# Kernel optimization log

Hardware: AMD Instinct MI355X
Metric: run time of the kernel (lower is better)

Reference implementation:

```python
import jax, jax.numpy as jnp
import numpy as np

B, C_IN, C_OUT, H, W = 8, 64, 64, 128, 128
G, K, PAD = 8, 3, 1
CG_OUT = C_OUT // G   # 8
CG_IN = C_IN // G     # 8


def setup_inputs() -> dict:
    key = jax.random.key(0)
    ks = jax.random.split(key, 6)
    x = jax.random.normal(ks[0], (B, C_IN, H, W), dtype=jnp.float32)
    # grouped 1x1 conv weights, stored as (groups, out_per_group, in_per_group)
    scale = (2.0 / C_OUT) ** 0.5  # kaiming fan_out
    Wq = jax.random.normal(ks[1], (G, CG_OUT, CG_IN), dtype=jnp.float32) * scale
    Wk = jax.random.normal(ks[2], (G, CG_OUT, CG_IN), dtype=jnp.float32) * scale
    Wv = jax.random.normal(ks[3], (G, CG_OUT, CG_IN), dtype=jnp.float32) * scale
    h_emb = jax.random.normal(ks[4], (G, CG_OUT // 2, 1, 1, K, 1), dtype=jnp.float32)
    w_emb = jax.random.normal(ks[5], (G, CG_OUT // 2, 1, 1, 1, K), dtype=jnp.float32)
    return {"x": x, "Wq": Wq, "Wk": Wk, "Wv": Wv, "h_emb": h_emb, "w_emb": w_emb}


def _gconv1x1(x, Wt):
    # grouped 1x1 conv: x (B,C,H,W) -> (B,G,Cg,H,W)
    b, c, h, w = x.shape
    xg = x.reshape(b, G, c // G, h, w)
    return jnp.einsum('bgihw,goi->bgohw', xg, Wt)


def _unfold(t):
    # t: (B,G,Cg,H+2p,W+2p) -> (B,G,Cg,H,W,K*K), window index = i*K + j (h-major,
    # matching torch unfold(2).unfold(3).view)
    slices = [t[..., i:i + H, j:j + W] for i in range(K) for j in range(K)]
    return jnp.stack(slices, axis=-1)


def reference(x, Wq, Wk, Wv, h_emb, w_emb):
    x_pad = jnp.pad(x, ((0, 0), (0, 0), (PAD, PAD), (PAD, PAD)))
    q = _gconv1x1(x, Wq)            # (B,G,Cg,H,W)
    kf = _gconv1x1(x_pad, Wk)       # (B,G,Cg,H+2,W+2)
    vf = _gconv1x1(x_pad, Wv)
    kp = _unfold(kf)                # (B,G,Cg,H,W,K^2)
    vp = _unfold(vf)
    # relative position embedding: h half broadcast over w, w half over h
    he = jnp.broadcast_to(h_emb, (G, CG_OUT // 2, 1, 1, K, K))
    we = jnp.broadcast_to(w_emb, (G, CG_OUT // 2, 1, 1, K, K))
    emb = jnp.concatenate([he, we], axis=1).reshape(G, CG_OUT, 1, 1, K * K)
    logits = q[..., None] * (kp + emb[None])       # (B,G,Cg,H,W,K^2)
    attn = jax.nn.softmax(logits, axis=-1)
    out = jnp.sum(attn * vp, axis=-1)              # (B,G,Cg,H,W)
    return out.reshape(x.shape[0], C_OUT, H, W)
```

## Files before the change

### kernel.cpp

```cpp
#include <hip/hip_runtime.h>


typedef float v2f __attribute__((ext_vector_type(2)));
typedef float v4f __attribute__((ext_vector_type(4)));

#define HH 128
#define WW 128
#define HW (HH * WW)
#define PT 34
#define PTS 38
#define LOG2E 1.44269504088896f

__device__ __forceinline__ float sload(float v) {
    return __uint_as_float(__builtin_amdgcn_readfirstlane(__float_as_uint(v)));
}

__global__ __launch_bounds__(256, 5) void sab_fused(
    const float* __restrict__ x,
    const float* __restrict__ Wq,
    const float* __restrict__ Wk,
    const float* __restrict__ Wv,
    const float* __restrict__ h_emb,
    const float* __restrict__ w_emb,
    float* __restrict__ out)
{
    __shared__ v2f kv[2][PT][PTS];

    const int bid0 = blockIdx.x;
    const int work = (bid0 & 7) * 512 + (bid0 >> 3);
    const int c0   = (work & 3) << 1;
    const int tile = (work >> 2) & 15;
    const int bg   = work >> 6;
    const int g    = bg & 7;
    const int h0   = (tile >> 2) << 5;
    const int w0   = (tile & 3) << 5;
    const int tid  = threadIdx.x;
    const int ty   = tid >> 3;
    const int x0   = (tid & 7) << 2;

    float wk[2][8], wv[2][8], wq[2][8], eb[2][9];
    #pragma unroll
    for (int cc = 0; cc < 2; cc++) {
        const int c = c0 + cc;
        #pragma unroll
        for (int i = 0; i < 8; i++) {
            wk[cc][i] = sload(Wk[g * 64 + c * 8 + i]);
            wv[cc][i] = sload(Wv[g * 64 + c * 8 + i]);
            wq[cc][i] = sload(Wq[g * 64 + c * 8 + i]);
        }
        #pragma unroll
        for (int p = 0; p < 9; p++) {
            eb[cc][p] = sload((c < 4) ? h_emb[(g * 4 + c) * 3 + p / 3]
                                      : w_emb[(g * 4 + c - 4) * 3 + p % 3]);
        }
    }

    const float* xb = x + (size_t)bg * 8 * HW;
    const int ibase = (h0 + ty) * WW + (w0 + x0);

    v4f xi[8];
    #pragma unroll
    for (int i = 0; i < 8; i++)
        xi[i] = *reinterpret_cast<const v4f*>(xb + i * HW + ibase);

    v4f kk0 = 0.f, vv0 = 0.f, qq0 = 0.f, kk1 = 0.f, vv1 = 0.f, qq1 = 0.f;
    #pragma unroll
    for (int i = 0; i < 8; i++) {
        const v4f xv = xi[i];
        kk0 += wk[0][i] * xv;  vv0 += wv[0][i] * xv;  qq0 += wq[0][i] * xv;
        kk1 += wk[1][i] * xv;  vv1 += wv[1][i] * xv;  qq1 += wq[1][i] * xv;
    }
    #pragma unroll
    for (int px = 0; px < 4; px++) {
        kv[0][ty + 1][x0 + 1 + px] = (v2f){kk0[px], vv0[px]};
        kv[1][ty + 1][x0 + 1 + px] = (v2f){kk1[px], vv1[px]};
    }
    float q[2][4];
    #pragma unroll
    for (int px = 0; px < 4; px++) {
        q[0][px] = qq0[px] * LOG2E;
        q[1][px] = qq1[px] * LOG2E;
    }

    if (tid < 132) {
        int hpy, hpx;
        if (tid < 34)       { hpy = 0;        hpx = tid; }
        else if (tid < 68)  { hpy = 33;       hpx = tid - 34; }
        else if (tid < 100) { hpy = tid - 67; hpx = 0; }
        else                { hpy = tid - 99; hpx = 33; }
        const int gh = h0 + hpy - 1, gw = w0 + hpx - 1;
        const bool ok = (gh >= 0) & (gh < HH) & (gw >= 0) & (gw < WW);
        const int base = gh * WW + gw;
        float hk0 = 0.f, hv0 = 0.f, hk1 = 0.f, hv1 = 0.f;
        #pragma unroll
        for (int i = 0; i < 8; i++) {
            const float xv = ok ? xb[i * HW + base] : 0.0f;
            hk0 = fmaf(wk[0][i], xv, hk0);
            hv0 = fmaf(wv[0][i], xv, hv0);
            hk1 = fmaf(wk[1][i], xv, hk1);
            hv1 = fmaf(wv[1][i], xv, hv1);
        }
        kv[0][hpy][hpx] = (v2f){hk0, hv0};
        kv[1][hpy][hpx] = (v2f){hk1, hv1};
    }
    __syncthreads();

    float s[2][4] = {{0.f,0.f,0.f,0.f},{0.f,0.f,0.f,0.f}};
    float o[2][4] = {{0.f,0.f,0.f,0.f},{0.f,0.f,0.f,0.f}};
    #pragma unroll
    for (int dh = 0; dh < 3; dh++) {
        #pragma unroll
        for (int cc = 0; cc < 2; cc++) {
            const v2f* row = &kv[cc][ty + dh][x0];
            const v4f a  = *reinterpret_cast<const v4f*>(row);
            const v4f bq = *reinterpret_cast<const v4f*>(row + 2);
            const v4f cq = *reinterpret_cast<const v4f*>(row + 4);
            const float kw[6] = {a.x, a.z, bq.x, bq.z, cq.x, cq.z};
            const float vw[6] = {a.y, a.w, bq.y, bq.w, cq.y, cq.w};
            #pragma unroll
            for (int px = 0; px < 4; px++) {
                const float ql = q[cc][px];
                #pragma unroll
                for (int dw = 0; dw < 3; dw++) {
                    const float e = __builtin_amdgcn_exp2f(
                        ql * (kw[px + dw] + eb[cc][dh * 3 + dw]));
                    s[cc][px] += e;
                    o[cc][px] = fmaf(e, vw[px + dw], o[cc][px]);
                }
            }
        }
    }

    v4f r0, r1;
    #pragma unroll
    for (int px = 0; px < 4; px++) {
        r0[px] = o[0][px] * __builtin_amdgcn_rcpf(s[0][px]);
        r1[px] = o[1][px] * __builtin_amdgcn_rcpf(s[1][px]);
    }
    *reinterpret_cast<v4f*>(out + (size_t)(bg * 8 + c0 + 0) * HW + ibase) = r0;
    *reinterpret_cast<v4f*>(out + (size_t)(bg * 8 + c0 + 1) * HW + ibase) = r1;
}

extern "C" void kernel_launch(void* const* d_in, const int* in_sizes, int n_in,
                              void* d_out, int out_size, void* d_ws, size_t ws_size,
                              hipStream_t stream) {
    const float* x    = (const float*)d_in[0];
    const float* Wq   = (const float*)d_in[1];
    const float* Wk   = (const float*)d_in[2];
    const float* Wv   = (const float*)d_in[3];
    const float* h_e  = (const float*)d_in[4];
    const float* w_e  = (const float*)d_in[5];
    float* out = (float*)d_out;

    dim3 grid(8 * 8 * 16 * 4);
    dim3 block(256);
    sab_fused<<<grid, block, 0, stream>>>(x, Wq, Wk, Wv, h_e, w_e, out);
}
```

Baseline: 28.06 us.

## Use full-width 8-row tiles with planar K/V shared-memory layout

Changes each block's tile from 32x32 to 8 rows by the full 128-pixel width, so only top and bottom halo rows need recomputing and the left/right halo disappears (handled as zero padding at the image edge). K and V move from interleaved float2 to separate planar float arrays, so stores and center loads become 16-byte vectors and halo loads are coalesced v4f reads by 64 threads. The cost is a larger halo fraction per tile (2 rows per 8 instead of a ring per 32x32) and extra scalar LDS loads for the left and right neighbours.

```diff
diff --git a/kernel.cpp b/kernel.cpp
--- a/kernel.cpp
+++ b/kernel.cpp
@@ -1,14 +1,12 @@
 #include <hip/hip_runtime.h>
 
 
-typedef float v2f __attribute__((ext_vector_type(2)));
 typedef float v4f __attribute__((ext_vector_type(4)));
 
 #define HH 128
 #define WW 128
 #define HW (HH * WW)
-#define PT 34
-#define PTS 38
+#define LSTR 132
 #define LOG2E 1.44269504088896f
 
 __device__ __forceinline__ float sload(float v) {
@@ -24,7 +22,8 @@
     const float* __restrict__ w_emb,
     float* __restrict__ out)
 {
-    __shared__ v2f kv[2][PT][PTS];
+    __shared__ float kpl[2][10][LSTR];
+    __shared__ float vpl[2][10][LSTR];
 
     const int bid0 = blockIdx.x;
     const int work = (bid0 & 7) * 512 + (bid0 >> 3);
@@ -32,11 +31,10 @@
     const int tile = (work >> 2) & 15;
     const int bg   = work >> 6;
     const int g    = bg & 7;
-    const int h0   = (tile >> 2) << 5;
-    const int w0   = (tile & 3) << 5;
+    const int h0   = tile << 3;
     const int tid  = threadIdx.x;
-    const int ty   = tid >> 3;
-    const int x0   = (tid & 7) << 2;
+    const int ty   = tid >> 5;
+    const int x0   = (tid & 31) << 2;
 
     float wk[2][8], wv[2][8], wq[2][8], eb[2][9];
     #pragma unroll
@@ -56,7 +54,7 @@
     }
 
     const float* xb = x + (size_t)bg * 8 * HW;
-    const int ibase = (h0 + ty) * WW + (w0 + x0);
+    const int ibase = (h0 + ty) * WW + x0;
 
     v4f xi[8];
     #pragma unroll
@@ -70,56 +68,54 @@
         kk0 += wk[0][i] * xv;  vv0 += wv[0][i] * xv;  qq0 += wq[0][i] * xv;
         kk1 += wk[1][i] * xv;  vv1 += wv[1][i] * xv;  qq1 += wq[1][i] * xv;
     }
-    #pragma unroll
-    for (int px = 0; px < 4; px++) {
-        kv[0][ty + 1][x0 + 1 + px] = (v2f){kk0[px], vv0[px]};
-        kv[1][ty + 1][x0 + 1 + px] = (v2f){kk1[px], vv1[px]};
-    }
-    float q[2][4];
-    #pragma unroll
-    for (int px = 0; px < 4; px++) {
-        q[0][px] = qq0[px] * LOG2E;
-        q[1][px] = qq1[px] * LOG2E;
-    }
+    *reinterpret_cast<v4f*>(&kpl[0][ty + 1][x0]) = kk0;
+    *reinterpret_cast<v4f*>(&vpl[0][ty + 1][x0]) = vv0;
+    *reinterpret_cast<v4f*>(&kpl[1][ty + 1][x0]) = kk1;
+    *reinterpret_cast<v4f*>(&vpl[1][ty + 1][x0]) = vv1;
+    const v4f q0 = qq0 * LOG2E;
+    const v4f q1 = qq1 * LOG2E;
 
-    if (tid < 132) {
-        int hpy, hpx;
-        if (tid < 34)       { hpy = 0;        hpx = tid; }
-        else if (tid < 68)  { hpy = 33;       hpx = tid - 34; }
-        else if (tid < 100) { hpy = tid - 67; hpx = 0; }
-        else                { hpy = tid - 99; hpx = 33; }
-        const int gh = h0 + hpy - 1, gw = w0 + hpx - 1;
-        const bool ok = (gh >= 0) & (gh < HH) & (gw >= 0) & (gw < WW);
-        const int base = gh * WW + gw;
-        float hk0 = 0.f, hv0 = 0.f, hk1 = 0.f, hv1 = 0.f;
-        #pragma unroll
-        for (int i = 0; i < 8; i++) {
-            const float xv = ok ? xb[i * HW + base] : 0.0f;
-            hk0 = fmaf(wk[0][i], xv, hk0);
-            hv0 = fmaf(wv[0][i], xv, hv0);
-            hk1 = fmaf(wk[1][i], xv, hk1);
-            hv1 = fmaf(wv[1][i], xv, hv1);
+    if (tid < 64) {
+        const int hr  = tid >> 5;
+        const int hx0 = (tid & 31) << 2;
+        const int gh  = h0 - 1 + hr * 9;
+        const int lr  = hr * 9;
+        v4f hk0 = 0.f, hv0 = 0.f, hk1 = 0.f, hv1 = 0.f;
+        if (gh >= 0 && gh < HH) {
+            const int base = gh * WW + hx0;
+            #pragma unroll
+            for (int i = 0; i < 8; i++) {
+                const v4f xv = *reinterpret_cast<const v4f*>(xb + i * HW + base);
+                hk0 += wk[0][i] * xv;  hv0 += wv[0][i] * xv;
+                hk1 += wk[1][i] * xv;  hv1 += wv[1][i] * xv;
+            }
         }
-        kv[0][hpy][hpx] = (v2f){hk0, hv0};
-        kv[1][hpy][hpx] = (v2f){hk1, hv1};
+        *reinterpret_cast<v4f*>(&kpl[0][lr][hx0]) = hk0;
+        *reinterpret_cast<v4f*>(&vpl[0][lr][hx0]) = hv0;
+        *reinterpret_cast<v4f*>(&kpl[1][lr][hx0]) = hk1;
+        *reinterpret_cast<v4f*>(&vpl[1][lr][hx0]) = hv1;
     }
     __syncthreads();
 
     float s[2][4] = {{0.f,0.f,0.f,0.f},{0.f,0.f,0.f,0.f}};
     float o[2][4] = {{0.f,0.f,0.f,0.f},{0.f,0.f,0.f,0.f}};
+
     #pragma unroll
-    for (int dh = 0; dh < 3; dh++) {
+    for (int cc = 0; cc < 2; cc++) {
         #pragma unroll
-        for (int cc = 0; cc < 2; cc++) {
-            const v2f* row = &kv[cc][ty + dh][x0];
-            const v4f a  = *reinterpret_cast<const v4f*>(row);
-            const v4f bq = *reinterpret_cast<const v4f*>(row + 2);
-            const v4f cq = *reinterpret_cast<const v4f*>(row + 4);
-            const float kw[6] = {a.x, a.z, bq.x, bq.z, cq.x, cq.z};
-            const float vw[6] = {a.y, a.w, bq.y, bq.w, cq.y, cq.w};
+        for (int dh = 0; dh < 3; dh++) {
+            const int lr = ty + dh;
+            const v4f Bk = *reinterpret_cast<const v4f*>(&kpl[cc][lr][x0]);
+            const v4f Bv = *reinterpret_cast<const v4f*>(&vpl[cc][lr][x0]);
+            const float kL = x0        ? kpl[cc][lr][x0 - 1] : 0.f;
+            const float vL = x0        ? vpl[cc][lr][x0 - 1] : 0.f;
+            const float kR = (x0 < 124) ? kpl[cc][lr][x0 + 4] : 0.f;
+            const float vR = (x0 < 124) ? vpl[cc][lr][x0 + 4] : 0.f;
+            const float kw[6] = {kL, Bk.x, Bk.y, Bk.z, Bk.w, kR};
+            const float vw[6] = {vL, Bv.x, Bv.y, Bv.z, Bv.w, vR};
             #pragma unroll
             for (int px = 0; px < 4; px++) {
-                const float ql = q[cc][px];
+                const float ql = (cc ? q1 : q0)[px];
                 #pragma unroll
                 for (int dw = 0; dw < 3; dw++) {
                     const float e = __builtin_amdgcn_exp2f(
```

After: 82.44 us. 2.94x slower.

## Reshape spatial tile to 16x64 with vectorized halo-row computation

Applied to the files above, without the earlier changes.

Changes each block's spatial tile from 32x32 to 16 rows by 64 columns and resizes the shared K/V buffer to match. The top and bottom halo rows are now computed by 32 threads using float4 loads, and the side columns and corners are handled by 36 scalar threads, replacing the earlier 132-thread scalar halo path. The launch-bounds occupancy hint of 5 is removed. The aim is coalesced, vectorized halo loads with fewer divergent scalar accesses, in exchange for a larger halo perimeter per tile and possibly different register allocation now that the occupancy hint is gone.

```diff
diff --git a/kernel.cpp b/kernel.cpp
--- a/kernel.cpp
+++ b/kernel.cpp
@@ -7,15 +7,14 @@
 #define HH 128
 #define WW 128
 #define HW (HH * WW)
-#define PT 34
-#define PTS 38
+#define PTS 70
 #define LOG2E 1.44269504088896f
 
 __device__ __forceinline__ float sload(float v) {
     return __uint_as_float(__builtin_amdgcn_readfirstlane(__float_as_uint(v)));
 }
 
-__global__ __launch_bounds__(256, 5) void sab_fused(
+__global__ __launch_bounds__(256) void sab_fused(
     const float* __restrict__ x,
     const float* __restrict__ Wq,
     const float* __restrict__ Wk,
@@ -24,7 +23,7 @@
     const float* __restrict__ w_emb,
     float* __restrict__ out)
 {
-    __shared__ v2f kv[2][PT][PTS];
+    __shared__ v2f kv[2][18][PTS];
 
     const int bid0 = blockIdx.x;
     const int work = (bid0 & 7) * 512 + (bid0 >> 3);
@@ -32,11 +31,11 @@
     const int tile = (work >> 2) & 15;
     const int bg   = work >> 6;
     const int g    = bg & 7;
-    const int h0   = (tile >> 2) << 5;
-    const int w0   = (tile & 3) << 5;
+    const int h0   = (tile >> 1) << 4;
+    const int w0   = (tile & 1) << 6;
     const int tid  = threadIdx.x;
-    const int ty   = tid >> 3;
-    const int x0   = (tid & 7) << 2;
+    const int ty   = tid >> 4;
+    const int x0   = (tid & 15) << 2;
 
     float wk[2][8], wv[2][8], wq[2][8], eb[2][9];
     #pragma unroll
@@ -75,20 +74,42 @@
         kv[0][ty + 1][x0 + 1 + px] = (v2f){kk0[px], vv0[px]};
         kv[1][ty + 1][x0 + 1 + px] = (v2f){kk1[px], vv1[px]};
     }
-    float q[2][4];
-    #pragma unroll
-    for (int px = 0; px < 4; px++) {
-        q[0][px] = qq0[px] * LOG2E;
-        q[1][px] = qq1[px] * LOG2E;
-    }
+    const v4f q0 = qq0 * LOG2E;
+    const v4f q1 = qq1 * LOG2E;
 
-    if (tid < 132) {
-        int hpy, hpx;
-        if (tid < 34)       { hpy = 0;        hpx = tid; }
-        else if (tid < 68)  { hpy = 33;       hpx = tid - 34; }
-        else if (tid < 100) { hpy = tid - 67; hpx = 0; }
-        else                { hpy = tid - 99; hpx = 33; }
-        const int gh = h0 + hpy - 1, gw = w0 + hpx - 1;
+    if (tid < 32) {
+        const int hr  = tid >> 4;
+        const int t   = tid & 15;
+        const int gh  = hr ? (h0 + 16) : (h0 - 1);
+        const int lr  = hr ? 17 : 0;
+        const int gw  = w0 + (t << 2);
+        v4f hk0 = 0.f, hv0 = 0.f, hk1 = 0.f, hv1 = 0.f;
+        if (gh >= 0 && gh < HH) {
+            const int base = gh * WW + gw;
+            #pragma unroll
+            for (int i = 0; i < 8; i++) {
+                const v4f xv = *reinterpret_cast<const v4f*>(xb + i * HW + base);
+                hk0 += wk[0][i] * xv;  hv0 += wv[0][i] * xv;
+                hk1 += wk[1][i] * xv;  hv1 += wv[1][i] * xv;
+            }
+        }
+        #pragma unroll
+        for (int px = 0; px < 4; px++) {
+            kv[0][lr][1 + (t << 2) + px] = (v2f){hk0[px], hv0[px]};
+            kv[1][lr][1 + (t << 2) + px] = (v2f){hk1[px], hv1[px]};
+        }
+    } else if (tid < 68) {
+        int hpy, hpx, gh, gw;
+        if (tid < 48)      { hpy = 1 + (tid - 32); hpx = 0;  gh = h0 + (tid - 32); gw = w0 - 1; }
+        else if (tid < 64) { hpy = 1 + (tid - 48); hpx = 65; gh = h0 + (tid - 48); gw = w0 + 64; }
+        else {
+            const int t = tid - 64;
+            const int cy = t >> 1, cx = t & 1;
+            hpy = cy ? 17 : 0;
+            hpx = cx ? 65 : 0;
+            gh  = cy ? (h0 + 16) : (h0 - 1);
+            gw  = cx ? (w0 + 64) : (w0 - 1);
+        }
         const bool ok = (gh >= 0) & (gh < HH) & (gw >= 0) & (gw < WW);
         const int base = gh * WW + gw;
         float hk0 = 0.f, hv0 = 0.f, hk1 = 0.f, hv1 = 0.f;
@@ -119,7 +140,7 @@
             const float vw[6] = {a.y, a.w, bq.y, bq.w, cq.y, cq.w};
             #pragma unroll
             for (int px = 0; px < 4; px++) {
-                const float ql = q[cc][px];
+                const float ql = (cc ? q1 : q0)[px];
                 #pragma unroll
                 for (int dw = 0; dw < 3; dw++) {
                     const float e = __builtin_amdgcn_exp2f(
```

Result: slower. 30.78 us (+9.7%).

## Process four output channels per block with double-buffered k/v tiles

Applied to the files above, without the earlier changes.

Each block now handles four output channels instead of two, halving the grid. It reuses the loaded x tile and halo values across both channel pairs, so x reads from global memory are halved. The k/v computation for the second pair is interleaved with the softmax of the first pair through a double-buffered shared-memory tile. In exchange it uses twice the LDS, more registers, and drops the occupancy hint from launch bounds, which may reduce waves per CU.

```diff
diff --git a/kernel.cpp b/kernel.cpp
--- a/kernel.cpp
+++ b/kernel.cpp
@@ -7,7 +7,6 @@
 #define HH 128
 #define WW 128
 #define HW (HH * WW)
-#define PT 34
 #define PTS 38
 #define LOG2E 1.44269504088896f
 
@@ -15,7 +14,7 @@
     return __uint_as_float(__builtin_amdgcn_readfirstlane(__float_as_uint(v)));
 }
 
-__global__ __launch_bounds__(256, 5) void sab_fused(
+__global__ __launch_bounds__(256) void sab_fused(
     const float* __restrict__ x,
     const float* __restrict__ Wq,
     const float* __restrict__ Wk,
@@ -24,13 +23,13 @@
     const float* __restrict__ w_emb,
     float* __restrict__ out)
 {
-    __shared__ v2f kv[2][PT][PTS];
+    __shared__ v2f kv[2][2][34][PTS];
 
     const int bid0 = blockIdx.x;
-    const int work = (bid0 & 7) * 512 + (bid0 >> 3);
-    const int c0   = (work & 3) << 1;
-    const int tile = (work >> 2) & 15;
-    const int bg   = work >> 6;
+    const int work = (bid0 & 7) * 256 + (bid0 >> 3);
+    const int c0   = (work & 1) << 2;
+    const int tile = (work >> 1) & 15;
+    const int bg   = work >> 5;
     const int g    = bg & 7;
     const int h0   = (tile >> 2) << 5;
     const int w0   = (tile & 3) << 5;
@@ -38,107 +37,203 @@
     const int ty   = tid >> 3;
     const int x0   = (tid & 7) << 2;
 
-    float wk[2][8], wv[2][8], wq[2][8], eb[2][9];
+    const float* xb = x + (size_t)bg * 8 * HW;
+    const int ibase = (h0 + ty) * WW + (w0 + x0);
+
+    float wkA[2][8], wvA[2][8], wqA[2][8], ebA[2][9];
     #pragma unroll
     for (int cc = 0; cc < 2; cc++) {
         const int c = c0 + cc;
         #pragma unroll
         for (int i = 0; i < 8; i++) {
-            wk[cc][i] = sload(Wk[g * 64 + c * 8 + i]);
-            wv[cc][i] = sload(Wv[g * 64 + c * 8 + i]);
-            wq[cc][i] = sload(Wq[g * 64 + c * 8 + i]);
-        }
-        #pragma unroll
-        for (int p = 0; p < 9; p++) {
-            eb[cc][p] = sload((c < 4) ? h_emb[(g * 4 + c) * 3 + p / 3]
-                                      : w_emb[(g * 4 + c - 4) * 3 + p % 3]);
-        }
-    }
-
-    const float* xb = x + (size_t)bg * 8 * HW;
-    const int ibase = (h0 + ty) * WW + (w0 + x0);
+            wkA[cc][i] = sload(Wk[g * 64 + c * 8 + i]);
+            wvA[cc][i] = sload(Wv[g * 64 + c * 8 + i]);
+            wqA[cc][i] = sload(Wq[g * 64 + c * 8 + i]);
+        }
+        #pragma unroll
+        for (int p = 0; p < 9; p++)
+            ebA[cc][p] = sload((c < 4) ? h_emb[(g * 4 + c) * 3 + p / 3]
+                                       : w_emb[(g * 4 + c - 4) * 3 + p % 3]);
+    }
 
     v4f xi[8];
     #pragma unroll
     for (int i = 0; i < 8; i++)
         xi[i] = *reinterpret_cast<const v4f*>(xb + i * HW + ibase);
 
-    v4f kk0 = 0.f, vv0 = 0.f, qq0 = 0.f, kk1 = 0.f, vv1 = 0.f, qq1 = 0.f;
-    #pragma unroll
-    for (int i = 0; i < 8; i++) {
-        const v4f xv = xi[i];
-        kk0 += wk[0][i] * xv;  vv0 += wv[0][i] * xv;  qq0 += wq[0][i] * xv;
-        kk1 += wk[1][i] * xv;  vv1 += wv[1][i] * xv;  qq1 += wq[1][i] * xv;
-    }
-    #pragma unroll
-    for (int px = 0; px < 4; px++) {
-        kv[0][ty + 1][x0 + 1 + px] = (v2f){kk0[px], vv0[px]};
-        kv[1][ty + 1][x0 + 1 + px] = (v2f){kk1[px], vv1[px]};
-    }
-    float q[2][4];
-    #pragma unroll
-    for (int px = 0; px < 4; px++) {
-        q[0][px] = qq0[px] * LOG2E;
-        q[1][px] = qq1[px] * LOG2E;
-    }
-
-    if (tid < 132) {
-        int hpy, hpx;
+    int hpy = 0, hpx = 0;
+    const bool is_halo = tid < 132;
+    if (is_halo) {
         if (tid < 34)       { hpy = 0;        hpx = tid; }
         else if (tid < 68)  { hpy = 33;       hpx = tid - 34; }
         else if (tid < 100) { hpy = tid - 67; hpx = 0; }
         else                { hpy = tid - 99; hpx = 33; }
-        const int gh = h0 + hpy - 1, gw = w0 + hpx - 1;
-        const bool ok = (gh >= 0) & (gh < HH) & (gw >= 0) & (gw < WW);
-        const int base = gh * WW + gw;
-        float hk0 = 0.f, hv0 = 0.f, hk1 = 0.f, hv1 = 0.f;
+    }
+    const int hgh = h0 + hpy - 1, hgw = w0 + hpx - 1;
+    const bool hok = is_halo & (hgh >= 0) & (hgh < HH) & (hgw >= 0) & (hgw < WW);
+    const int hbase = hgh * WW + hgw;
+    float hx[8];
+    #pragma unroll
+    for (int i = 0; i < 8; i++)
+        hx[i] = hok ? xb[i * HW + hbase] : 0.0f;
+
+    float qA[2][4];
+    {
+        v4f kk0 = 0.f, vv0 = 0.f, qq0 = 0.f, kk1 = 0.f, vv1 = 0.f, qq1 = 0.f;
         #pragma unroll
         for (int i = 0; i < 8; i++) {
-            const float xv = ok ? xb[i * HW + base] : 0.0f;
-            hk0 = fmaf(wk[0][i], xv, hk0);
-            hv0 = fmaf(wv[0][i], xv, hv0);
-            hk1 = fmaf(wk[1][i], xv, hk1);
-            hv1 = fmaf(wv[1][i], xv, hv1);
-        }
-        kv[0][hpy][hpx] = (v2f){hk0, hv0};
-        kv[1][hpy][hpx] = (v2f){hk1, hv1};
+            const v4f xv = xi[i];
+            kk0 += wkA[0][i] * xv;  vv0 += wvA[0][i] * xv;  qq0 += wqA[0][i] * xv;
+            kk1 += wkA[1][i] * xv;  vv1 += wvA[1][i] * xv;  qq1 += wqA[1][i] * xv;
+        }
+        #pragma unroll
+        for (int px = 0; px < 4; px++) {
+            kv[0][0][ty + 1][x0 + 1 + px] = (v2f){kk0[px], vv0[px]};
+            kv[0][1][ty + 1][x0 + 1 + px] = (v2f){kk1[px], vv1[px]};
+        }
+        #pragma unroll
+        for (int px = 0; px < 4; px++) {
+            qA[0][px] = qq0[px] * LOG2E;
+            qA[1][px] = qq1[px] * LOG2E;
+        }
+        if (is_halo) {
+            float hk0 = 0.f, hv0 = 0.f, hk1 = 0.f, hv1 = 0.f;
+            #pragma unroll
+            for (int i = 0; i < 8; i++) {
+                hk0 = fmaf(wkA[0][i], hx[i], hk0);
+                hv0 = fmaf(wvA[0][i], hx[i], hv0);
+                hk1 = fmaf(wkA[1][i], hx[i], hk1);
+                hv1 = fmaf(wvA[1][i], hx[i], hv1);
+            }
+            kv[0][0][hpy][hpx] = (v2f){hk0, hv0};
+            kv[0][1][hpy][hpx] = (v2f){hk1, hv1};
+        }
     }
     __syncthreads();
 
-    float s[2][4] = {{0.f,0.f,0.f,0.f},{0.f,0.f,0.f,0.f}};
-    float o[2][4] = {{0.f,0.f,0.f,0.f},{0.f,0.f,0.f,0.f}};
-    #pragma unroll
-    for (int dh = 0; dh < 3; dh++) {
+    float qB[2][4];
+    {
+        float wkB[2][8], wvB[2][8], wqB[2][8];
         #pragma unroll
         for (int cc = 0; cc < 2; cc++) {
-            const v2f* row = &kv[cc][ty + dh][x0];
-            const v4f a  = *reinterpret_cast<const v4f*>(row);
-            const v4f bq = *reinterpret_cast<const v4f*>(row + 2);
-            const v4f cq = *reinterpret_cast<const v4f*>(row + 4);
-            const float kw[6] = {a.x, a.z, bq.x, bq.z, cq.x, cq.z};
-            const float vw[6] = {a.y, a.w, bq.y, bq.w, cq.y, cq.w};
-            #pragma unroll
-            for (int px = 0; px < 4; px++) {
-                const float ql = q[cc][px];
+            const int c = c0 + 2 + cc;
+            #pragma unroll
+            for (int i = 0; i < 8; i++) {
+                wkB[cc][i] = sload(Wk[g * 64 + c * 8 + i]);
+                wvB[cc][i] = sload(Wv[g * 64 + c * 8 + i]);
+                wqB[cc][i] = sload(Wq[g * 64 + c * 8 + i]);
+            }
+        }
+        v4f kk0 = 0.f, vv0 = 0.f, qq0 = 0.f, kk1 = 0.f, vv1 = 0.f, qq1 = 0.f;
+        #pragma unroll
+        for (int i = 0; i < 8; i++) {
+            const v4f xv = xi[i];
+            kk0 += wkB[0][i] * xv;  vv0 += wvB[0][i] * xv;  qq0 += wqB[0][i] * xv;
+            kk1 += wkB[1][i] * xv;  vv1 += wvB[1][i] * xv;  qq1 += wqB[1][i] * xv;
+        }
+        #pragma unroll
+        for (int px = 0; px < 4; px++) {
+            kv[1][0][ty + 1][x0 + 1 + px] = (v2f){kk0[px], vv0[px]};
+            kv[1][1][ty + 1][x0 + 1 + px] = (v2f){kk1[px], vv1[px]};
+        }
+        #pragma unroll
+        for (int px = 0; px < 4; px++) {
+            qB[0][px] = qq0[px] * LOG2E;
+            qB[1][px] = qq1[px] * LOG2E;
+        }
+        if (is_halo) {
+            float hk0 = 0.f, hv0 = 0.f, hk1 = 0.f, hv1 = 0.f;
+            #pragma unroll
+            for (int i = 0; i < 8; i++) {
+                hk0 = fmaf(wkB[0][i], hx[i], hk0);
+                hv0 = fmaf(wvB[0][i], hx[i], hv0);
+                hk1 = fmaf(wkB[1][i], hx[i], hk1);
+                hv1 = fmaf(wvB[1][i], hx[i], hv1);
+            }
+            kv[1][0][hpy][hpx] = (v2f){hk0, hv0};
+            kv[1][1][hpy][hpx] = (v2f){hk1, hv1};
+        }
+
+        float s[2][4] = {{0.f,0.f,0.f,0.f},{0.f,0.f,0.f,0.f}};
+        float o[2][4] = {{0.f,0.f,0.f,0.f},{0.f,0.f,0.f,0.f}};
+        #pragma unroll
+        for (int dh = 0; dh < 3; dh++) {
+            #pragma unroll
+            for (int cc = 0; cc < 2; cc++) {
+                const v2f* row = &kv[0][cc][ty + dh][x0];
+                const v4f a  = *reinterpret_cast<const v4f*>(row);
+                const v4f bq = *reinterpret_cast<const v4f*>(row + 2);
+                const v4f cq = *reinterpret_cast<const v4f*>(row + 4);
+                const float kw[6] = {a.x, a.z, bq.x, bq.z, cq.x, cq.z};
+                const float vw[6] = {a.y, a.w, bq.y, bq.w, cq.y, cq.w};
                 #pragma unroll
-                for (int dw = 0; dw < 3; dw++) {
-                    const float e = __builtin_amdgcn_exp2f(
-                        ql * (kw[px + dw] + eb[cc][dh * 3 + dw]));
-                    s[cc][px] += e;
-                    o[cc][px] = fmaf(e, vw[px + dw], o[cc][px]);
+                for (int px = 0; px < 4; px++) {
+                    const float ql = qA[cc][px];
+                    #pragma unroll
+                    for (int dw = 0; dw < 3; dw++) {
+                        const float e = __builtin_amdgcn_exp2f(
+                            ql * (kw[px + dw] + ebA[cc][dh * 3 + dw]));
+                        s[cc][px] += e;
+                        o[cc][px] = fmaf(e, vw[px + dw], o[cc][px]);
+                    }
                 }
             }
         }
-    }
-
-    v4f r0, r1;
-    #pragma unroll
-    for (int px = 0; px < 4; px++) {
-        r0[px] = o[0][px] * __builtin_amdgcn_rcpf(s[0][px]);
-        r1[px] = o[1][px] * __builtin_amdgcn_rcpf(s[1][px]);
-    }
-    *reinterpret_cast<v4f*>(out + (size_t)(bg * 8 + c0 + 0) * HW + ibase) = r0;
-    *reinterpret_cast<v4f*>(out + (size_t)(bg * 8 + c0 + 1) * HW + ibase) = r1;
+        v4f r0, r1;
+        #pragma unroll
+        for (int px = 0; px < 4; px++) {
+            r0[px] = o[0][px] * __builtin_amdgcn_rcpf(s[0][px]);
+            r1[px] = o[1][px] * __builtin_amdgcn_rcpf(s[1][px]);
+        }
+        *reinterpret_cast<v4f*>(out + (size_t)(bg * 8 + c0 + 0) * HW + ibase) = r0;
+        *reinterpret_cast<v4f*>(out + (size_t)(bg * 8 + c0 + 1) * HW + ibase) = r1;
+    }
+    __syncthreads();
+
+    {
+        float ebB[2][9];
+        #pragma unroll
+        for (int cc = 0; cc < 2; cc++) {
+            const int c = c0 + 2 + cc;
+            #pragma unroll
+            for (int p = 0; p < 9; p++)
+                ebB[cc][p] = sload((c < 4) ? h_emb[(g * 4 + c) * 3 + p / 3]
+                                           : w_emb[(g * 4 + c - 4) * 3 + p % 3]);
+        }
+        float s[2][4] = {{0.f,0.f,0.f,0.f},{0.f,0.f,0.f,0.f}};
+        float o[2][4] = {{0.f,0.f,0.f,0.f},{0.f,0.f,0.f,0.f}};
+        #pragma unroll
+        for (int dh = 0; dh < 3; dh++) {
+            #pragma unroll
+            for (int cc = 0; cc < 2; cc++) {
+                const v2f* row = &kv[1][cc][ty + dh][x0];
+                const v4f a  = *reinterpret_cast<const v4f*>(row);
+                const v4f bq = *reinterpret_cast<const v4f*>(row + 2);
+                const v4f cq = *reinterpret_cast<const v4f*>(row + 4);
+                const float kw[6] = {a.x, a.z, bq.x, bq.z, cq.x, cq.z};
+                const float vw[6] = {a.y, a.w, bq.y, bq.w, cq.y, cq.w};
+                #pragma unroll
+                for (int px = 0; px < 4; px++) {
+                    const float ql = qB[cc][px];
+                    #pragma unroll
+                    for (int dw = 0; dw < 3; dw++) {
+                        const float e = __builtin_amdgcn_exp2f(
+                            ql * (kw[px + dw] + ebB[cc][dh * 3 + dw]));
+                        s[cc][px] += e;
+                        o[cc][px] = fmaf(e, vw[px + dw], o[cc][px]);
+                    }
+                }
+            }
+        }
+        v4f r0, r1;
+        #pragma unroll
+        for (int px = 0; px < 4; px++) {
+            r0[px] = o[0][px] * __builtin_amdgcn_rcpf(s[0][px]);
+            r1[px] = o[1][px] * __builtin_amdgcn_rcpf(s[1][px]);
+        }
+        *reinterpret_cast<v4f*>(out + (size_t)(bg * 8 + c0 + 2) * HW + ibase) = r0;
+        *reinterpret_cast<v4f*>(out + (size_t)(bg * 8 + c0 + 3) * HW + ibase) = r1;
+    }
 }
 
 extern "C" void kernel_launch(void* const* d_in, const int* in_sizes, int n_in,
@@ -152,7 +247,7 @@
     const float* w_e  = (const float*)d_in[5];
     float* out = (float*)d_out;
 
-    dim3 grid(8 * 8 * 16 * 4);
+    dim3 grid(8 * 8 * 16 * 2);
     dim3 block(256);
     sab_fused<<<grid, block, 0, stream>>>(x, Wq, Wk, Wv, h_e, w_e, out);
 }
```

Result: slower. 31.01 us (+10.5%).
